# Kernel optimization log

Measured on AMD Instinct MI355X. Metric: run time of the kernel, lower is better.

Reference implementation:

```python
import jax, jax.numpy as jnp
import numpy as np

N_NODES = 100000
N_EDGES = 1600000
N_GRAPHS = 1000
X_S = 128
HID = 64


def setup_inputs() -> dict:
    key = jax.random.key(0)
    ks = jax.random.split(key, 12)
    x = jax.random.normal(ks[0], (N_NODES, X_S), dtype=jnp.float32)
    edge_index = jax.random.randint(ks[1], (2, N_EDGES), 0, N_NODES, dtype=jnp.int64)
    batch = jnp.sort(jax.random.randint(ks[2], (N_NODES,), 0, N_GRAPHS, dtype=jnp.int64))
    def lin(k, fin, fout):
        s = 1.0 / np.sqrt(fin)
        kw, kb = jax.random.split(k)
        W = jax.random.uniform(kw, (fin, fout), minval=-s, maxval=s, dtype=jnp.float32)
        b = jax.random.uniform(kb, (fout,), minval=-s, maxval=s, dtype=jnp.float32)
        return W, b
    W1, b1 = lin(ks[3], X_S, HID)
    W2, b2 = lin(ks[4], HID, HID)
    W3, b3 = lin(ks[5], HID, HID)
    Wf, bf = lin(ks[6], HID, 10)
    Wl, bl = lin(ks[7], 10, 1)
    eps1 = jnp.float32(0.37)
    eps2 = jnp.float32(0.72)
    eps3 = jnp.float32(0.11)
    return {"x": x, "edge_index": edge_index, "batch": batch,
            "W1": W1, "b1": b1, "W2": W2, "b2": b2, "W3": W3, "b3": b3,
            "Wf": Wf, "bf": bf, "Wl": Wl, "bl": bl,
            "eps1": eps1, "eps2": eps2, "eps3": eps3}


def _gin_conv(h, src, dst, eps, W, b):
    # GIN: nn((1+eps)*x_i + sum_{j in N(i)} x_j); messages flow src -> dst
    agg = jax.ops.segment_sum(h[src], dst, num_segments=N_NODES)  # [N, d]
    return ((1.0 + eps) * h + agg) @ W + b


def reference(x, edge_index, batch, W1, b1, W2, b2, W3, b3, Wf, bf, Wl, bl,
              eps1, eps2, eps3):
    src, dst = edge_index[0], edge_index[1]
    h = jax.nn.relu(_gin_conv(x, src, dst, eps1, W1, b1))
    h = jax.nn.relu(_gin_conv(h, src, dst, eps2, W2, b2))
    h = jax.nn.relu(_gin_conv(h, src, dst, eps3, W3, b3))
    # global_mean_pool over graph ids
    sums = jax.ops.segment_sum(h, batch, num_segments=N_GRAPHS)        # [G, 64]
    cnts = jax.ops.segment_sum(jnp.ones((N_NODES,), h.dtype), batch,
                               num_segments=N_GRAPHS)                   # [G]
    pooled = sums / jnp.maximum(cnts, 1.0)[:, None]
    out = jax.nn.relu(pooled @ Wf + bf) @ Wl + bl                       # [G, 1]
    return out
```

## Files before the change

kernel.cpp:

```cpp
#include <hip/hip_runtime.h>

#define N_NODES 100000
#define N_EDGES 1600000
#define N_GRAPHS 1000

#define NB_C 782
#define B1   256
#define CHUNK (N_EDGES / B1)
#define MTOT (NB_C * B1)

#define LSTR 68

typedef unsigned int uint32;
typedef unsigned short ushort16;

static __device__ __forceinline__ ushort16 f2bf(float f) {
    uint32 u = __float_as_uint(f);
    u += 0x7fffu + ((u >> 16) & 1u);
    return (ushort16)(u >> 16);
}
static __device__ __forceinline__ void bf2x(uint32 v, float& lo, float& hi) {
    lo = __uint_as_float(v << 16);
    hi = __uint_as_float(v & 0xffff0000u);
}


__global__ __launch_bounds__(256) void count_kernel(
    const int* __restrict__ dst, int* __restrict__ M)
{
    __shared__ int cnt[NB_C];
    int b = blockIdx.x, t = threadIdx.x;
    for (int q = t; q < NB_C; q += 256) cnt[q] = 0;
    __syncthreads();
    int e0 = b * CHUNK;
    for (int e = e0 + t; e < e0 + CHUNK; e += 256)
        atomicAdd(&cnt[dst[e] >> 7], 1);
    __syncthreads();
    for (int q = t; q < NB_C; q += 256) M[q * B1 + b] = cnt[q];
}

#define SCAN_B 1024
#define SCAN_NBLK ((MTOT + SCAN_B - 1) / SCAN_B)

__global__ __launch_bounds__(256) void scanA_kernel(
    const int* __restrict__ in, int* __restrict__ excl, int* __restrict__ bsum)
{
    __shared__ int s[256];
    int b = blockIdx.x, t = threadIdx.x;
    int base = b * SCAN_B + t * 4;
    int v[4];
#pragma unroll
    for (int i = 0; i < 4; ++i) v[i] = (base + i < MTOT) ? in[base + i] : 0;
    int tsum = v[0] + v[1] + v[2] + v[3];
    s[t] = tsum;
    __syncthreads();
    for (int off = 1; off < 256; off <<= 1) {
        int x = (t >= off) ? s[t - off] : 0;
        __syncthreads();
        s[t] += x;
        __syncthreads();
    }
    int run = s[t] - tsum;
#pragma unroll
    for (int i = 0; i < 4; ++i) {
        if (base + i < MTOT) excl[base + i] = run;
        run += v[i];
    }
    if (t == 255) bsum[b] = s[255];
}

__global__ __launch_bounds__(256) void scanB_kernel(int* __restrict__ bsum)
{
    __shared__ int s[256];
    int t = threadIdx.x;
    int v = (t < SCAN_NBLK) ? bsum[t] : 0;
    s[t] = v;
    __syncthreads();
    for (int off = 1; off < 256; off <<= 1) {
        int x = (t >= off) ? s[t - off] : 0;
        __syncthreads();
        s[t] += x;
        __syncthreads();
    }
    if (t < SCAN_NBLK) bsum[t] = s[t] - v;
}

__global__ __launch_bounds__(256) void scanC_kernel(
    const int* __restrict__ excl, const int* __restrict__ bsum,
    int* __restrict__ out)
{
    int b = blockIdx.x, t = threadIdx.x;
    int add = bsum[b];
    int base = b * SCAN_B + t * 4;
#pragma unroll
    for (int i = 0; i < 4; ++i)
        if (base + i < MTOT) out[base + i] = excl[base + i] + add;
}

__global__ __launch_bounds__(256) void scatter_kernel(
    const int* __restrict__ src, const int* __restrict__ dst,
    const int* __restrict__ Ms, uint32* __restrict__ tmp)
{
    __shared__ int cur[NB_C];
    int b = blockIdx.x, t = threadIdx.x;
    for (int q = t; q < NB_C; q += 256) cur[q] = Ms[q * B1 + b];
    __syncthreads();
    int e0 = b * CHUNK;
    for (int e = e0 + t; e < e0 + CHUNK; e += 256) {
        int d = dst[e];
        int q = d >> 7;
        int pos = atomicAdd(&cur[q], 1);
        tmp[pos] = ((uint32)(d & 127) << 17) | (uint32)src[e];
    }
}

__global__ __launch_bounds__(256) void finalize_kernel(
    const uint32* __restrict__ tmp, const int* __restrict__ Ms,
    int* __restrict__ row_off, int* __restrict__ esrc)
{
    __shared__ int cnt[128];
    __shared__ int pref[128];
    __shared__ int cur[128];
    int q = blockIdx.x, t = threadIdx.x;
    int start = Ms[q * B1];
    int end = (q == NB_C - 1) ? N_EDGES : Ms[(q + 1) * B1];

    if (t < 128) cnt[t] = 0;
    __syncthreads();
    for (int e = start + t; e < end; e += 256)
        atomicAdd(&cnt[tmp[e] >> 17], 1);
    __syncthreads();
    if (t < 128) pref[t] = cnt[t];
    __syncthreads();
    for (int off = 1; off < 128; off <<= 1) {
        int x = 0;
        if (t < 128 && t >= off) x = pref[t - off];
        __syncthreads();
        if (t < 128) pref[t] += x;
        __syncthreads();
    }
    if (t < 128) {
        int excl = pref[t] - cnt[t];
        int node = q * 128 + t;
        if (node < N_NODES) row_off[node] = start + excl;
        cur[t] = start + excl;
    }
    if (q == 0 && t == 0) row_off[N_NODES] = N_EDGES;
    __syncthreads();
    for (int e = start + t; e < end; e += 256) {
        uint32 u = tmp[e];
        int pos = atomicAdd(&cur[u >> 17], 1);
        esrc[pos] = (int)(u & 0x1FFFFu);
    }
}

template<int IN>
__global__ __launch_bounds__(256) void gemm_kernel(
    const float* __restrict__ h,
    const float* __restrict__ W,
    ushort16* __restrict__ y)
{
    __shared__ float hs[64 * LSTR];
    __shared__ float wsh[64 * 64];

    const int t = threadIdx.x;
    const int node0 = blockIdx.x * 64;
    const int m = t >> 4;
    const int p = t & 15;

    float4 acc[4];
#pragma unroll
    for (int i = 0; i < 4; ++i) acc[i] = make_float4(0.f, 0.f, 0.f, 0.f);

    for (int kb = 0; kb < IN / 64; ++kb) {
        if (kb) __syncthreads();
        {
            int kc = (t & 15) * 4;
            int rbase = t >> 4;
#pragma unroll
            for (int rr = 0; rr < 4; ++rr) {
                int row = rr * 16 + rbase;
                int node = node0 + row;
                float4 v = make_float4(0.f, 0.f, 0.f, 0.f);
                if (node < N_NODES)
                    v = *(const float4*)&h[(size_t)node * IN + kb * 64 + kc];
                *(float4*)&hs[row * LSTR + kc] = v;
            }
        }
        {
            int j4 = (t & 15) * 4;
            int kbase = t >> 4;
#pragma unroll
            for (int it = 0; it < 4; ++it) {
                int k = it * 16 + kbase;
                *(float4*)&wsh[k * 64 + j4] =
                    *(const float4*)&W[(size_t)(kb * 64 + k) * 64 + j4];
            }
        }
        __syncthreads();

        const float* hb = &hs[(m * 4) * LSTR];
#pragma unroll 4
        for (int kc = 0; kc < 64; kc += 4) {
            float4 hv[4];
#pragma unroll
            for (int i = 0; i < 4; ++i) hv[i] = *(const float4*)&hb[i * LSTR + kc];
            float4 w0 = *(const float4*)&wsh[(kc + 0) * 64 + p * 4];
            float4 w1 = *(const float4*)&wsh[(kc + 1) * 64 + p * 4];
            float4 w2 = *(const float4*)&wsh[(kc + 2) * 64 + p * 4];
            float4 w3 = *(const float4*)&wsh[(kc + 3) * 64 + p * 4];
#pragma unroll
            for (int i = 0; i < 4; ++i) {
                acc[i].x = fmaf(hv[i].x, w0.x, acc[i].x);
                acc[i].y = fmaf(hv[i].x, w0.y, acc[i].y);
                acc[i].z = fmaf(hv[i].x, w0.z, acc[i].z);
                acc[i].w = fmaf(hv[i].x, w0.w, acc[i].w);
                acc[i].x = fmaf(hv[i].y, w1.x, acc[i].x);
                acc[i].y = fmaf(hv[i].y, w1.y, acc[i].y);
                acc[i].z = fmaf(hv[i].y, w1.z, acc[i].z);
                acc[i].w = fmaf(hv[i].y, w1.w, acc[i].w);
                acc[i].x = fmaf(hv[i].z, w2.x, acc[i].x);
                acc[i].y = fmaf(hv[i].z, w2.y, acc[i].y);
                acc[i].z = fmaf(hv[i].z, w2.z, acc[i].z);
                acc[i].w = fmaf(hv[i].z, w2.w, acc[i].w);
                acc[i].x = fmaf(hv[i].w, w3.x, acc[i].x);
                acc[i].y = fmaf(hv[i].w, w3.y, acc[i].y);
                acc[i].z = fmaf(hv[i].w, w3.z, acc[i].z);
                acc[i].w = fmaf(hv[i].w, w3.w, acc[i].w);
            }
        }
    }

#pragma unroll
    for (int i = 0; i < 4; ++i) {
        int node = node0 + m * 4 + i;
        if (node >= N_NODES) continue;
        uint32 w0 = (uint32)f2bf(acc[i].x) | ((uint32)f2bf(acc[i].y) << 16);
        uint32 w1 = (uint32)f2bf(acc[i].z) | ((uint32)f2bf(acc[i].w) << 16);
        *(uint2*)&y[(size_t)node * 64 + p * 4] = make_uint2(w0, w1);
    }
}

__global__ __launch_bounds__(256) void aggregate_kernel(
    const uint32* __restrict__ y,
    const int* __restrict__ row_off,
    const int* __restrict__ esrc,
    const float* __restrict__ b,
    const float* __restrict__ eps_p,
    float* __restrict__ out)
{
    int node = blockIdx.x * 4 + (threadIdx.x >> 6);
    int lane = threadIdx.x & 63;
    int j = lane >> 3;
    int w = lane & 7;
    if (node >= N_NODES) return;

    int s0 = row_off[node], s1 = row_off[node + 1];
    float a[8], c[8];
#pragma unroll
    for (int i = 0; i < 8; ++i) { a[i] = 0.f; c[i] = 0.f; }

    const uint32* yw = y + (size_t)w * 4;
    int e = s0 + j;
    for (; e + 8 < s1; e += 16) {
        int i0 = esrc[e];
        int i1 = esrc[e + 8];
        uint4 v0 = *(const uint4*)&yw[(size_t)i0 * 32];
        uint4 v1 = *(const uint4*)&yw[(size_t)i1 * 32];
        float lo, hi;
        bf2x(v0.x, lo, hi); a[0] += lo; a[1] += hi;
        bf2x(v0.y, lo, hi); a[2] += lo; a[3] += hi;
        bf2x(v0.z, lo, hi); a[4] += lo; a[5] += hi;
        bf2x(v0.w, lo, hi); a[6] += lo; a[7] += hi;
        bf2x(v1.x, lo, hi); c[0] += lo; c[1] += hi;
        bf2x(v1.y, lo, hi); c[2] += lo; c[3] += hi;
        bf2x(v1.z, lo, hi); c[4] += lo; c[5] += hi;
        bf2x(v1.w, lo, hi); c[6] += lo; c[7] += hi;
    }
    if (e < s1) {
        int i0 = esrc[e];
        uint4 v0 = *(const uint4*)&yw[(size_t)i0 * 32];
        float lo, hi;
        bf2x(v0.x, lo, hi); a[0] += lo; a[1] += hi;
        bf2x(v0.y, lo, hi); a[2] += lo; a[3] += hi;
        bf2x(v0.z, lo, hi); a[4] += lo; a[5] += hi;
        bf2x(v0.w, lo, hi); a[6] += lo; a[7] += hi;
    }
#pragma unroll
    for (int i = 0; i < 8; ++i) {
        a[i] += c[i];
        a[i] += __shfl_xor(a[i], 8);
        a[i] += __shfl_xor(a[i], 16);
        a[i] += __shfl_xor(a[i], 32);
    }

    uint4 sv = *(const uint4*)&yw[(size_t)node * 32];
    float s[8];
    bf2x(sv.x, s[0], s[1]);
    bf2x(sv.y, s[2], s[3]);
    bf2x(sv.z, s[4], s[5]);
    bf2x(sv.w, s[6], s[7]);
    float ep1 = 1.0f + eps_p[0];
    float4 b0 = *(const float4*)&b[w * 8];
    float4 b1 = *(const float4*)&b[w * 8 + 4];
    float r[8];
    r[0] = fmaxf(fmaf(ep1, s[0], a[0]) + b0.x, 0.0f);
    r[1] = fmaxf(fmaf(ep1, s[1], a[1]) + b0.y, 0.0f);
    r[2] = fmaxf(fmaf(ep1, s[2], a[2]) + b0.z, 0.0f);
    r[3] = fmaxf(fmaf(ep1, s[3], a[3]) + b0.w, 0.0f);
    r[4] = fmaxf(fmaf(ep1, s[4], a[4]) + b1.x, 0.0f);
    r[5] = fmaxf(fmaf(ep1, s[5], a[5]) + b1.y, 0.0f);
    r[6] = fmaxf(fmaf(ep1, s[6], a[6]) + b1.z, 0.0f);
    r[7] = fmaxf(fmaf(ep1, s[7], a[7]) + b1.w, 0.0f);
    if (j == 0) {
        float* o = &out[(size_t)node * 64 + w * 8];
        *(float4*)o       = make_float4(r[0], r[1], r[2], r[3]);
        *(float4*)(o + 4) = make_float4(r[4], r[5], r[6], r[7]);
    }
}

__global__ __launch_bounds__(256) void pool_head_kernel(
    const float* __restrict__ h,
    const int* __restrict__ batch,
    const float* __restrict__ Wf,
    const float* __restrict__ bfv,
    const float* __restrict__ Wl,
    const float* __restrict__ blv,
    float* __restrict__ out)
{
    __shared__ float red[4][64];
    __shared__ float pooled[64];
    __shared__ float hid[10];
    int g = blockIdx.x;
    int t = threadIdx.x;
    int lo = 0, hi = N_NODES;
    while (lo < hi) { int mid = (lo + hi) >> 1; if (batch[mid] < g) lo = mid + 1; else hi = mid; }
    int start = lo;
    hi = N_NODES;
    while (lo < hi) { int mid = (lo + hi) >> 1; if (batch[mid] < g + 1) lo = mid + 1; else hi = mid; }
    int end = lo;

    int c = t & 63, nl = t >> 6;
    float acc = 0.0f;
    for (int i = start + nl; i < end; i += 4) acc += h[i * 64 + c];
    red[nl][c] = acc;
    __syncthreads();
    if (t < 64) {
        float cnt = (float)(end - start);
        float inv = 1.0f / fmaxf(cnt, 1.0f);
        pooled[t] = (red[0][t] + red[1][t] + red[2][t] + red[3][t]) * inv;
    }
    __syncthreads();
    if (t < 10) {
        float s = bfv[t];
#pragma unroll
        for (int k = 0; k < 64; ++k) s = fmaf(pooled[k], Wf[k * 10 + t], s);
        hid[t] = fmaxf(s, 0.0f);
    }
    __syncthreads();
    if (t == 0) {
        float s = blv[0];
#pragma unroll
        for (int j = 0; j < 10; ++j) s = fmaf(hid[j], Wl[j], s);
        out[g] = s;
    }
}

extern "C" void kernel_launch(void* const* d_in, const int* in_sizes, int n_in,
                              void* d_out, int out_size, void* d_ws, size_t ws_size,
                              hipStream_t stream)
{
    const float* x     = (const float*)d_in[0];
    const int*   ei    = (const int*)  d_in[1];
    const int*   src   = ei;
    const int*   dst   = ei + N_EDGES;
    const int*   batch = (const int*)  d_in[2];
    const float* W1    = (const float*)d_in[3];
    const float* b1    = (const float*)d_in[4];
    const float* W2    = (const float*)d_in[5];
    const float* b2    = (const float*)d_in[6];
    const float* W3    = (const float*)d_in[7];
    const float* b3    = (const float*)d_in[8];
    const float* Wf    = (const float*)d_in[9];
    const float* bfv   = (const float*)d_in[10];
    const float* Wl    = (const float*)d_in[11];
    const float* blv   = (const float*)d_in[12];
    const float* eps1  = (const float*)d_in[13];
    const float* eps2  = (const float*)d_in[14];
    const float* eps3  = (const float*)d_in[15];

    ushort16* ybf = (ushort16*)d_ws;
    float* h1   = (float*)(ybf + (size_t)N_NODES * 64);
    float* h2   = h1 + (size_t)N_NODES * 64;
    int*   ints = (int*)(h2 + (size_t)N_NODES * 64);
    int*   M       = ints;
    int*   Mex     = M + MTOT;
    int*   Ms      = Mex + MTOT;
    int*   bsum    = Ms + MTOT;
    int*   row_off = bsum + 256;
    int*   esrc    = row_off + N_NODES + 1;
    uint32* tmp    = (uint32*)(esrc + N_EDGES);

    count_kernel<<<B1, 256, 0, stream>>>(dst, M);
    scanA_kernel<<<SCAN_NBLK, 256, 0, stream>>>(M, Mex, bsum);
    scanB_kernel<<<1, 256, 0, stream>>>(bsum);
    scanC_kernel<<<SCAN_NBLK, 256, 0, stream>>>(Mex, bsum, Ms);
    scatter_kernel<<<B1, 256, 0, stream>>>(src, dst, Ms, tmp);
    finalize_kernel<<<NB_C, 256, 0, stream>>>(tmp, Ms, row_off, esrc);

    const int gemm_blk = (N_NODES + 63) / 64;
    const int agg_blk  = (N_NODES + 3) / 4;

    gemm_kernel<128><<<gemm_blk, 256, 0, stream>>>(x, W1, ybf);
    aggregate_kernel<<<agg_blk, 256, 0, stream>>>((const uint32*)ybf, row_off, esrc, b1, eps1, h1);

    gemm_kernel<64><<<gemm_blk, 256, 0, stream>>>(h1, W2, ybf);
    aggregate_kernel<<<agg_blk, 256, 0, stream>>>((const uint32*)ybf, row_off, esrc, b2, eps2, h2);

    gemm_kernel<64><<<gemm_blk, 256, 0, stream>>>(h2, W3, ybf);
    aggregate_kernel<<<agg_blk, 256, 0, stream>>>((const uint32*)ybf, row_off, esrc, b3, eps3, h1);

    pool_head_kernel<<<N_GRAPHS, 256, 0, stream>>>(h1, batch, Wf, bfv, Wl, blv,
                                                   (float*)d_out);
}
```

Measured before the change: 375.9 us.

## Fuse aggregation of layers 1-2 with the following layer's GEMM

Adds a kernel that aggregates the neighbour sums for 64 nodes into shared memory, applies eps, bias and ReLU, then multiplies by the next layer's weight matrix and writes bf16 output. This removes the fp32 intermediate h1/h2 round trip through global memory and two kernel launches. Two bf16 buffers ping-pong between layers. The trade-off is larger shared memory per block (about 33 KB), which lowers occupancy, and fewer blocks for the latency-bound gather phase. Each wave now handles 16 nodes serially instead of one block per 4 nodes.

```diff
diff --git a/kernel.cpp b/kernel.cpp
--- a/kernel.cpp
+++ b/kernel.cpp
@@ -241,6 +241,154 @@
     }
 }
 
+__global__ __launch_bounds__(256) void fused_agg_gemm_kernel(
+    const uint32* __restrict__ y,
+    const int* __restrict__ row_off,
+    const int* __restrict__ esrc,
+    const float* __restrict__ bprev,
+    const float* __restrict__ eps_p,
+    const float* __restrict__ W,
+    ushort16* __restrict__ yout)
+{
+    __shared__ float t[64 * LSTR];
+    __shared__ float wsh[64 * 64];
+
+    const int tid = threadIdx.x;
+    const int node0 = blockIdx.x * 64;
+    const int wv = tid >> 6;
+    const int lane = tid & 63;
+    const int j = lane >> 3;
+    const int w = lane & 7;
+
+    {
+        int j4 = (tid & 15) * 4;
+        int kbase = tid >> 4;
+#pragma unroll
+        for (int it = 0; it < 4; ++it) {
+            int k = it * 16 + kbase;
+            *(float4*)&wsh[k * 64 + j4] = *(const float4*)&W[(size_t)k * 64 + j4];
+        }
+    }
+
+    const float ep1 = 1.0f + eps_p[0];
+    const float4 b0 = *(const float4*)&bprev[w * 8];
+    const float4 b1v = *(const float4*)&bprev[w * 8 + 4];
+    const uint32* yw = y + (size_t)w * 4;
+
+    for (int n = 0; n < 16; ++n) {
+        int nl = wv * 16 + n;
+        int node = node0 + nl;
+        if (node < N_NODES) {
+            int s0 = row_off[node], s1 = row_off[node + 1];
+            float a[8], c[8];
+#pragma unroll
+            for (int i = 0; i < 8; ++i) { a[i] = 0.f; c[i] = 0.f; }
+            int e = s0 + j;
+            for (; e + 8 < s1; e += 16) {
+                int i0 = esrc[e];
+                int i1 = esrc[e + 8];
+                uint4 v0 = *(const uint4*)&yw[(size_t)i0 * 32];
+                uint4 v1 = *(const uint4*)&yw[(size_t)i1 * 32];
+                float lo, hi;
+                bf2x(v0.x, lo, hi); a[0] += lo; a[1] += hi;
+                bf2x(v0.y, lo, hi); a[2] += lo; a[3] += hi;
+                bf2x(v0.z, lo, hi); a[4] += lo; a[5] += hi;
+                bf2x(v0.w, lo, hi); a[6] += lo; a[7] += hi;
+                bf2x(v1.x, lo, hi); c[0] += lo; c[1] += hi;
+                bf2x(v1.y, lo, hi); c[2] += lo; c[3] += hi;
+                bf2x(v1.z, lo, hi); c[4] += lo; c[5] += hi;
+                bf2x(v1.w, lo, hi); c[6] += lo; c[7] += hi;
+            }
+            if (e < s1) {
+                int i0 = esrc[e];
+                uint4 v0 = *(const uint4*)&yw[(size_t)i0 * 32];
+                float lo, hi;
+                bf2x(v0.x, lo, hi); a[0] += lo; a[1] += hi;
+                bf2x(v0.y, lo, hi); a[2] += lo; a[3] += hi;
+                bf2x(v0.z, lo, hi); a[4] += lo; a[5] += hi;
+                bf2x(v0.w, lo, hi); a[6] += lo; a[7] += hi;
+            }
+#pragma unroll
+            for (int i = 0; i < 8; ++i) {
+                a[i] += c[i];
+                a[i] += __shfl_xor(a[i], 8);
+                a[i] += __shfl_xor(a[i], 16);
+                a[i] += __shfl_xor(a[i], 32);
+            }
+            uint4 sv = *(const uint4*)&yw[(size_t)node * 32];
+            float s[8];
+            bf2x(sv.x, s[0], s[1]);
+            bf2x(sv.y, s[2], s[3]);
+            bf2x(sv.z, s[4], s[5]);
+            bf2x(sv.w, s[6], s[7]);
+            if (j == 0) {
+                float r0 = fmaxf(fmaf(ep1, s[0], a[0]) + b0.x, 0.0f);
+                float r1 = fmaxf(fmaf(ep1, s[1], a[1]) + b0.y, 0.0f);
+                float r2 = fmaxf(fmaf(ep1, s[2], a[2]) + b0.z, 0.0f);
+                float r3 = fmaxf(fmaf(ep1, s[3], a[3]) + b0.w, 0.0f);
+                float r4 = fmaxf(fmaf(ep1, s[4], a[4]) + b1v.x, 0.0f);
+                float r5 = fmaxf(fmaf(ep1, s[5], a[5]) + b1v.y, 0.0f);
+                float r6 = fmaxf(fmaf(ep1, s[6], a[6]) + b1v.z, 0.0f);
+                float r7 = fmaxf(fmaf(ep1, s[7], a[7]) + b1v.w, 0.0f);
+                float* o = &t[nl * LSTR + w * 8];
+                *(float4*)o       = make_float4(r0, r1, r2, r3);
+                *(float4*)(o + 4) = make_float4(r4, r5, r6, r7);
+            }
+        } else if (j == 0) {
+            float* o = &t[nl * LSTR + w * 8];
+            *(float4*)o       = make_float4(0.f, 0.f, 0.f, 0.f);
+            *(float4*)(o + 4) = make_float4(0.f, 0.f, 0.f, 0.f);
+        }
+    }
+    __syncthreads();
+
+    const int m = tid >> 4;
+    const int p = tid & 15;
+    float4 acc[4];
+#pragma unroll
+    for (int i = 0; i < 4; ++i) acc[i] = make_float4(0.f, 0.f, 0.f, 0.f);
+
+    const float* hb = &t[(m * 4) * LSTR];
+#pragma unroll 4
+    for (int kc = 0; kc < 64; kc += 4) {
+        float4 hv[4];
+#pragma unroll
+        for (int i = 0; i < 4; ++i) hv[i] = *(const float4*)&hb[i * LSTR + kc];
+        float4 w0 = *(const float4*)&wsh[(kc + 0) * 64 + p * 4];
+        float4 w1 = *(const float4*)&wsh[(kc + 1) * 64 + p * 4];
+        float4 w2 = *(const float4*)&wsh[(kc + 2) * 64 + p * 4];
+        float4 w3 = *(const float4*)&wsh[(kc + 3) * 64 + p * 4];
+#pragma unroll
+        for (int i = 0; i < 4; ++i) {
+            acc[i].x = fmaf(hv[i].x, w0.x, acc[i].x);
+            acc[i].y = fmaf(hv[i].x, w0.y, acc[i].y);
+            acc[i].z = fmaf(hv[i].x, w0.z, acc[i].z);
+            acc[i].w = fmaf(hv[i].x, w0.w, acc[i].w);
+            acc[i].x = fmaf(hv[i].y, w1.x, acc[i].x);
+            acc[i].y = fmaf(hv[i].y, w1.y, acc[i].y);
+            acc[i].z = fmaf(hv[i].y, w1.z, acc[i].z);
+            acc[i].w = fmaf(hv[i].y, w1.w, acc[i].w);
+            acc[i].x = fmaf(hv[i].z, w2.x, acc[i].x);
+            acc[i].y = fmaf(hv[i].z, w2.y, acc[i].y);
+            acc[i].z = fmaf(hv[i].z, w2.z, acc[i].z);
+            acc[i].w = fmaf(hv[i].z, w2.w, acc[i].w);
+            acc[i].x = fmaf(hv[i].w, w3.x, acc[i].x);
+            acc[i].y = fmaf(hv[i].w, w3.y, acc[i].y);
+            acc[i].z = fmaf(hv[i].w, w3.z, acc[i].z);
+            acc[i].w = fmaf(hv[i].w, w3.w, acc[i].w);
+        }
+    }
+
+#pragma unroll
+    for (int i = 0; i < 4; ++i) {
+        int node = node0 + m * 4 + i;
+        if (node >= N_NODES) continue;
+        uint32 w0 = (uint32)f2bf(acc[i].x) | ((uint32)f2bf(acc[i].y) << 16);
+        uint32 w1 = (uint32)f2bf(acc[i].z) | ((uint32)f2bf(acc[i].w) << 16);
+        *(uint2*)&yout[(size_t)node * 64 + p * 4] = make_uint2(w0, w1);
+    }
+}
+
 __global__ __launch_bounds__(256) void aggregate_kernel(
     const uint32* __restrict__ y,
     const int* __restrict__ row_off,
@@ -303,19 +451,18 @@
     float ep1 = 1.0f + eps_p[0];
     float4 b0 = *(const float4*)&b[w * 8];
     float4 b1 = *(const float4*)&b[w * 8 + 4];
-    float r[8];
-    r[0] = fmaxf(fmaf(ep1, s[0], a[0]) + b0.x, 0.0f);
-    r[1] = fmaxf(fmaf(ep1, s[1], a[1]) + b0.y, 0.0f);
-    r[2] = fmaxf(fmaf(ep1, s[2], a[2]) + b0.z, 0.0f);
-    r[3] = fmaxf(fmaf(ep1, s[3], a[3]) + b0.w, 0.0f);
-    r[4] = fmaxf(fmaf(ep1, s[4], a[4]) + b1.x, 0.0f);
-    r[5] = fmaxf(fmaf(ep1, s[5], a[5]) + b1.y, 0.0f);
-    r[6] = fmaxf(fmaf(ep1, s[6], a[6]) + b1.z, 0.0f);
-    r[7] = fmaxf(fmaf(ep1, s[7], a[7]) + b1.w, 0.0f);
     if (j == 0) {
+        float r0 = fmaxf(fmaf(ep1, s[0], a[0]) + b0.x, 0.0f);
+        float r1 = fmaxf(fmaf(ep1, s[1], a[1]) + b0.y, 0.0f);
+        float r2 = fmaxf(fmaf(ep1, s[2], a[2]) + b0.z, 0.0f);
+        float r3 = fmaxf(fmaf(ep1, s[3], a[3]) + b0.w, 0.0f);
+        float r4 = fmaxf(fmaf(ep1, s[4], a[4]) + b1.x, 0.0f);
+        float r5 = fmaxf(fmaf(ep1, s[5], a[5]) + b1.y, 0.0f);
+        float r6 = fmaxf(fmaf(ep1, s[6], a[6]) + b1.z, 0.0f);
+        float r7 = fmaxf(fmaf(ep1, s[7], a[7]) + b1.w, 0.0f);
         float* o = &out[(size_t)node * 64 + w * 8];
-        *(float4*)o       = make_float4(r[0], r[1], r[2], r[3]);
-        *(float4*)(o + 4) = make_float4(r[4], r[5], r[6], r[7]);
+        *(float4*)o       = make_float4(r0, r1, r2, r3);
+        *(float4*)(o + 4) = make_float4(r4, r5, r6, r7);
     }
 }
 
@@ -389,10 +536,10 @@
     const float* eps2  = (const float*)d_in[14];
     const float* eps3  = (const float*)d_in[15];
 
-    ushort16* ybf = (ushort16*)d_ws;
-    float* h1   = (float*)(ybf + (size_t)N_NODES * 64);
-    float* h2   = h1 + (size_t)N_NODES * 64;
-    int*   ints = (int*)(h2 + (size_t)N_NODES * 64);
+    ushort16* ybA = (ushort16*)d_ws;
+    ushort16* ybB = ybA + (size_t)N_NODES * 64;
+    float* h3   = (float*)(ybB + (size_t)N_NODES * 64);
+    int*   ints = (int*)(h3 + (size_t)N_NODES * 64);
     int*   M       = ints;
     int*   Mex     = M + MTOT;
     int*   Ms      = Mex + MTOT;
@@ -411,15 +558,17 @@
     const int gemm_blk = (N_NODES + 63) / 64;
     const int agg_blk  = (N_NODES + 3) / 4;
 
-    gemm_kernel<128><<<gemm_blk, 256, 0, stream>>>(x, W1, ybf);
-    aggregate_kernel<<<agg_blk, 256, 0, stream>>>((const uint32*)ybf, row_off, esrc, b1, eps1, h1);
-
-    gemm_kernel<64><<<gemm_blk, 256, 0, stream>>>(h1, W2, ybf);
-    aggregate_kernel<<<agg_blk, 256, 0, stream>>>((const uint32*)ybf, row_off, esrc, b2, eps2, h2);
-
-    gemm_kernel<64><<<gemm_blk, 256, 0, stream>>>(h2, W3, ybf);
-    aggregate_kernel<<<agg_blk, 256, 0, stream>>>((const uint32*)ybf, row_off, esrc, b3, eps3, h1);
-
-    pool_head_kernel<<<N_GRAPHS, 256, 0, stream>>>(h1, batch, Wf, bfv, Wl, blv,
+    gemm_kernel<128><<<gemm_blk, 256, 0, stream>>>(x, W1, ybA);
+
+    fused_agg_gemm_kernel<<<gemm_blk, 256, 0, stream>>>(
+        (const uint32*)ybA, row_off, esrc, b1, eps1, W2, ybB);
+
+    fused_agg_gemm_kernel<<<gemm_blk, 256, 0, stream>>>(
+        (const uint32*)ybB, row_off, esrc, b2, eps2, W3, ybA);
+
+    aggregate_kernel<<<agg_blk, 256, 0, stream>>>(
+        (const uint32*)ybA, row_off, esrc, b3, eps3, h3);
+
+    pool_head_kernel<<<N_GRAPHS, 256, 0, stream>>>(h3, batch, Wf, bfv, Wl, blv,
                                                    (float*)d_out);
 }
```

Result: slower. 478.3 us (+27.2%).
